# Kernel tuning notes

Hardware: AMD Instinct MI355X
Metric: run time of the kernel (lower is better)

The kernel has to match this reference:

```python
import jax, jax.numpy as jnp
import numpy as np

NG, NPG, EPG = 64, 256, 2048        # graphs, nodes/graph, edges/graph
N, E = NG * NPG, NG * EPG
FN, FE, FG = 256, 64, 128           # node/edge/global feature dims
MSG_DIMS = [FE + 2 * FN + FG, 512, 512, 256]   # message_arch '512-512-256'
UPD_DIMS = [256 + FN + FG, 512, 256]           # node_arch '512-256'
N_EMB_G, OUT_NODE, OUT_ACT = 256, 64, 8


def _mlp(x, params):
    # Linear -> ReLU stack (Dropout is identity in eval mode)
    for w, b in params:
        x = jax.nn.relu(x @ w + b)
    return x


def setup_inputs():
    key = jax.random.key(0)
    ks = jax.random.split(key, 24)
    nodes = jax.random.normal(ks[0], (N, FN), jnp.float32)
    edge_attr = jax.random.normal(ks[1], (E, FE), jnp.float32)
    global_attr = jax.random.normal(ks[2], (NG, FG), jnp.float32)
    # edges are grouped by graph (matches repeat_interleave(global, num_edges))
    rng = np.random.default_rng(0)
    gid_e = np.repeat(np.arange(NG), EPG)
    src = gid_e * NPG + rng.integers(0, NPG, E)
    tgt = gid_e * NPG + rng.integers(0, NPG, E)
    edge_indices = jnp.asarray(np.stack([src, tgt]), jnp.int32)
    num_nodes = jnp.full((NG,), NPG, jnp.int32)
    num_edges = jnp.full((NG,), EPG, jnp.int32)
    batch_indices = jnp.asarray(np.repeat(np.arange(NG), NPG), jnp.int32)

    def lin(k, fi, fo):
        kw, kb = jax.random.split(k)
        lim = 1.0 / np.sqrt(fi)
        return (jax.random.uniform(kw, (fi, fo), jnp.float32, -lim, lim),
                jax.random.uniform(kb, (fo,), jnp.float32, -lim, lim))

    inp = dict(nodes=nodes, edge_attr=edge_attr, global_attr=global_attr,
               edge_indices=edge_indices, num_nodes=num_nodes,
               num_edges=num_edges, batch_indices=batch_indices)
    for i in range(3):
        w, b = lin(ks[3 + i], MSG_DIMS[i], MSG_DIMS[i + 1])
        inp[f'msg_w{i}'], inp[f'msg_b{i}'] = w, b
    for i in range(2):
        w, b = lin(ks[6 + i], UPD_DIMS[i], UPD_DIMS[i + 1])
        inp[f'upd_w{i}'], inp[f'upd_b{i}'] = w, b
    inp['glob_w'], inp['glob_b'] = lin(ks[8], UPD_DIMS[-1] + FG, N_EMB_G)
    inp['emb_w'], inp['emb_b'] = lin(ks[9], UPD_DIMS[-1], OUT_NODE)
    inp['act_w'], inp['act_b'] = lin(ks[10], N_EMB_G, OUT_ACT)
    return inp


def reference(nodes, edge_attr, global_attr, edge_indices, num_nodes,
              num_edges, batch_indices, msg_w0, msg_b0, msg_w1, msg_b1,
              msg_w2, msg_b2, upd_w0, upd_b0, upd_w1, upd_b1,
              glob_w, glob_b, emb_w, emb_b, act_w, act_b):
    n, e = nodes.shape[0], edge_indices.shape[1]
    ng = global_attr.shape[0]
    src, tgt = edge_indices[0], edge_indices[1]
    glob_e = jnp.repeat(global_attr, num_edges, axis=0, total_repeat_length=e)
    concat = jnp.concatenate([nodes[src], edge_attr, nodes[tgt], glob_e], axis=1)
    # message_nn ends with ReLU; outer F.relu is a no-op on non-neg values
    message = _mlp(concat, [(msg_w0, msg_b0), (msg_w1, msg_b1), (msg_w2, msg_b2)])
    # scatter_max into per-node slots; messages >= 0 so zeros init matches fill=0
    aggr = jnp.zeros((n, message.shape[1]), message.dtype).at[tgt].max(message)
    glob_n = jnp.repeat(global_attr, num_nodes, axis=0, total_repeat_length=n)
    h = _mlp(jnp.concatenate([nodes, aggr, glob_n], axis=1),
             [(upd_w0, upd_b0), (upd_w1, upd_b1)])
    agg_nodes = jnp.zeros((ng, h.shape[1]), h.dtype).at[batch_indices].max(h)
    g = jax.nn.relu(jnp.concatenate([agg_nodes, global_attr], axis=1) @ glob_w + glob_b)
    node_pred = jax.nn.relu(h @ emb_w + emb_b)
    action = jax.nn.softmax(g @ act_w + act_b, axis=1)
    return node_pred, action
```

## Files before the change

kernel.cpp:

```cpp
#include <hip/hip_runtime.h>
#include <hip/hip_bf16.h>

typedef unsigned short u16;
using u16x4 = __attribute__((ext_vector_type(4))) unsigned short;
using u16x8 = __attribute__((ext_vector_type(8))) unsigned short;
using u32x4 = __attribute__((ext_vector_type(4))) unsigned int;
using f32x4 = __attribute__((ext_vector_type(4))) float;
using bf16x8 = __attribute__((ext_vector_type(8))) __bf16;

#define TNG 64
#define TNN 16384
#define TNE 131072
#define TFN 256
#define TFE 64
#define TFG 128

__device__ __forceinline__ u16 f2bf(float f) {
    unsigned u = __float_as_uint(f);
    unsigned r = (u + 0x7FFFu + ((u >> 16) & 1u)) >> 16;
    return (u16)r;
}
__device__ __forceinline__ float b2f(u16 h) {
    return __uint_as_float(((unsigned)h) << 16);
}

__device__ __forceinline__ void gload_lds16(const u16* g, u16* l) {
    __builtin_amdgcn_global_load_lds(
        (const __attribute__((address_space(1))) void*)g,
        (__attribute__((address_space(3))) void*)l, 16, 0, 0);
}

__device__ __forceinline__ int xcd_swz(int bid, int nwg) {
    return (nwg & 7) == 0 ? (bid & 7) * (nwg >> 3) + (bid >> 3) : bid;
}


__global__ void cast_kernel(const float* __restrict__ in, u16* __restrict__ out, int n4) {
    int i = blockIdx.x * 256 + threadIdx.x;
    if (i >= n4) return;
    f32x4 v = *(const f32x4*)(in + (size_t)i * 4);
    u16x4 o;
    o.x = f2bf(v.x); o.y = f2bf(v.y); o.z = f2bf(v.z); o.w = f2bf(v.w);
    *(u16x4*)(out + (size_t)i * 4) = o;
}


struct PrepTab {
    const float* W[8];
    int out_off[8];
    int Nin[8], Nact[8], r0[8], Ksub[8];
    int tile0[8];
    int tkn[8];
};

__global__ __launch_bounds__(256) void prep_weights_kernel(PrepTab tab, u16* __restrict__ wsbase) {
    const int b = blockIdx.x;
    int i = 7;
#pragma unroll
    for (int j = 7; j > 0; --j)
        if (b < tab.tile0[j]) i = j - 1;
    const int loc = b - tab.tile0[i];
    const int tk = loc % tab.tkn[i];
    const int tn = loc / tab.tkn[i];
    const int kb = tk * 64, nb = tn * 64;
    const int Nin = tab.Nin[i], Nact = tab.Nact[i], r0 = tab.r0[i], Ksub = tab.Ksub[i];
    const float* W = tab.W[i];
    u16* outp = wsbase + tab.out_off[i];

    __shared__ float t[64][65];
    const int tid = threadIdx.x;
    const int nl = tid & 63;
    const bool nok = (nb + nl) < Nact;
#pragma unroll 4
    for (int kk = tid >> 6; kk < 64; kk += 4) {
        float v = nok ? W[(size_t)(r0 + kb + kk) * Nin + nb + nl] : 0.0f;
        t[kk][nl] = v;
    }
    __syncthreads();
    const int kl = tid & 63;
#pragma unroll 4
    for (int nn = tid >> 6; nn < 64; nn += 4)
        outp[(size_t)(nb + nn) * Ksub + kb + kl] = f2bf(t[kl][nn]);
}


template <int K, int NXSH, bool RELU, bool OUT_BF16>
__global__ __launch_bounds__(256) void gemm_bt_kernel(
    const u16* __restrict__ A, const u16* __restrict__ Bt,
    const float* __restrict__ bias, void* __restrict__ Cv,
    int Nout, int ldc) {
    constexpr int NT = K / 32;
    __shared__ u16 As[4][4096];
    __shared__ u16 Bs[4][4096];
    const int w = xcd_swz(blockIdx.x, gridDim.x);
    const int bxi = w & ((1 << NXSH) - 1);
    const int byi = w >> NXSH;
    const int tid = threadIdx.x;
    const int wave = tid >> 6, lane = tid & 63;
    const int wr = wave >> 1, wc = wave & 1;
    const size_t brow = (size_t)byi * 128;
    const size_t bcol = (size_t)bxi * 128;
    const int srow = tid >> 2;
    const int qsrc = (tid & 3) ^ ((srow >> 1) & 3);
    const u16* aSrc = A + (brow + srow) * (size_t)K + qsrc * 8;
    const u16* bSrc = Bt + (bcol + srow) * (size_t)K + qsrc * 8;
    const size_t stepRows = (size_t)64 * K;

    auto stage = [&](int t, int buf) {
        const int k0 = t * 32;
        gload_lds16(aSrc + k0, &As[buf][tid * 8]);
        gload_lds16(aSrc + stepRows + k0, &As[buf][tid * 8 + 2048]);
        gload_lds16(bSrc + k0, &Bs[buf][tid * 8]);
        gload_lds16(bSrc + stepRows + k0, &Bs[buf][tid * 8 + 2048]);
    };

    f32x4 acc[4][4] = {};

    stage(0, 0);
    stage(1, 1);
    stage(2, 2);
#pragma unroll
    for (int t = 0; t < NT; ++t) {
        const int cur = t & 3;
        if (t + 2 < NT)      asm volatile("s_waitcnt vmcnt(8)" ::: "memory");
        else if (t + 1 < NT) asm volatile("s_waitcnt vmcnt(4)" ::: "memory");
        else                 asm volatile("s_waitcnt vmcnt(0)" ::: "memory");
        __builtin_amdgcn_s_barrier();
        if (t + 3 < NT) stage(t + 3, (t + 3) & 3);
        bf16x8 af[4], bfv[4];
#pragma unroll
        for (int m = 0; m < 4; ++m) {
            const int row = wr * 64 + m * 16 + (lane & 15);
            const int slot = (lane >> 4) ^ ((row >> 1) & 3);
            af[m] = *(const bf16x8*)&As[cur][row * 32 + slot * 8];
        }
#pragma unroll
        for (int n = 0; n < 4; ++n) {
            const int row = wc * 64 + n * 16 + (lane & 15);
            const int slot = (lane >> 4) ^ ((row >> 1) & 3);
            bfv[n] = *(const bf16x8*)&Bs[cur][row * 32 + slot * 8];
        }
#pragma unroll
        for (int m = 0; m < 4; ++m)
#pragma unroll
            for (int n = 0; n < 4; ++n)
                acc[m][n] = __builtin_amdgcn_mfma_f32_16x16x32_bf16(af[m], bfv[n], acc[m][n], 0, 0, 0);
    }

    const int rowSub = wr * 64 + (lane >> 4) * 4;
#pragma unroll
    for (int n = 0; n < 4; ++n) {
        const int col = (int)bcol + wc * 64 + n * 16 + (lane & 15);
        if (col >= Nout) continue;
        const float bv = bias ? bias[col] : 0.0f;
#pragma unroll
        for (int m = 0; m < 4; ++m) {
#pragma unroll
            for (int i = 0; i < 4; ++i) {
                float v = acc[m][n][i] + bv;
                if (RELU) v = fmaxf(v, 0.0f);
                size_t off = (brow + rowSub + m * 16 + i) * (size_t)ldc + col;
                if (OUT_BF16) ((u16*)Cv)[off] = f2bf(v);
                else ((float*)Cv)[off] = v;
            }
        }
    }
}


__global__ __launch_bounds__(256) void gemm_u0_kernel(
    const u16* __restrict__ nodes_bf, const u16* __restrict__ aggr,
    const u16* __restrict__ glob_bf, const u16* __restrict__ U0T,
    const float* __restrict__ bias, u16* __restrict__ C) {
    constexpr int NT = 20;
    __shared__ u16 As[4][4096];
    __shared__ u16 Bs[4][4096];
    const int w = xcd_swz(blockIdx.x, gridDim.x);
    const int bxi = w & 3;
    const int byi = w >> 2;
    const int tid = threadIdx.x;
    const int wave = tid >> 6, lane = tid & 63;
    const int wr = wave >> 1, wc = wave & 1;
    const size_t brow = (size_t)byi * 128;
    const size_t bcol = (size_t)bxi * 128;
    const int srow = tid >> 2;
    const int scol = ((tid & 3) ^ ((srow >> 1) & 3)) * 8;
    const int r0i = (int)brow + srow;
    const u16* bSrc = U0T + (bcol + srow) * (size_t)640 + scol;

    auto stage = [&](int t, int buf) {
        const int k0 = t * 32;
        const u16 *p0, *p1;
        if (k0 < 256) {
            p0 = nodes_bf + (size_t)r0i * 256 + k0 + scol;
            p1 = nodes_bf + (size_t)(r0i + 64) * 256 + k0 + scol;
        } else if (k0 < 512) {
            p0 = aggr + (size_t)r0i * 256 + (k0 - 256) + scol;
            p1 = aggr + (size_t)(r0i + 64) * 256 + (k0 - 256) + scol;
        } else {
            p0 = glob_bf + (size_t)(r0i >> 8) * 128 + (k0 - 512) + scol;
            p1 = glob_bf + (size_t)((r0i + 64) >> 8) * 128 + (k0 - 512) + scol;
        }
        gload_lds16(p0, &As[buf][tid * 8]);
        gload_lds16(p1, &As[buf][tid * 8 + 2048]);
        gload_lds16(bSrc + k0, &Bs[buf][tid * 8]);
        gload_lds16(bSrc + (size_t)64 * 640 + k0, &Bs[buf][tid * 8 + 2048]);
    };

    f32x4 acc[4][4] = {};

    stage(0, 0);
    stage(1, 1);
    stage(2, 2);
#pragma unroll
    for (int t = 0; t < NT; ++t) {
        const int cur = t & 3;
        if (t + 2 < NT)      asm volatile("s_waitcnt vmcnt(8)" ::: "memory");
        else if (t + 1 < NT) asm volatile("s_waitcnt vmcnt(4)" ::: "memory");
        else                 asm volatile("s_waitcnt vmcnt(0)" ::: "memory");
        __builtin_amdgcn_s_barrier();
        if (t + 3 < NT) stage(t + 3, (t + 3) & 3);
        bf16x8 af[4], bfv[4];
#pragma unroll
        for (int m = 0; m < 4; ++m) {
            const int row = wr * 64 + m * 16 + (lane & 15);
            const int slot = (lane >> 4) ^ ((row >> 1) & 3);
            af[m] = *(const bf16x8*)&As[cur][row * 32 + slot * 8];
        }
#pragma unroll
        for (int n = 0; n < 4; ++n) {
            const int row = wc * 64 + n * 16 + (lane & 15);
            const int slot = (lane >> 4) ^ ((row >> 1) & 3);
            bfv[n] = *(const bf16x8*)&Bs[cur][row * 32 + slot * 8];
        }
#pragma unroll
        for (int m = 0; m < 4; ++m)
#pragma unroll
            for (int n = 0; n < 4; ++n)
                acc[m][n] = __builtin_amdgcn_mfma_f32_16x16x32_bf16(af[m], bfv[n], acc[m][n], 0, 0, 0);
    }

    const int rowSub = wr * 64 + (lane >> 4) * 4;
#pragma unroll
    for (int n = 0; n < 4; ++n) {
        const int col = (int)bcol + wc * 64 + n * 16 + (lane & 15);
        const float bv = bias[col];
#pragma unroll
        for (int m = 0; m < 4; ++m)
#pragma unroll
            for (int i = 0; i < 4; ++i) {
                float v = fmaxf(acc[m][n][i] + bv, 0.0f);
                C[(brow + rowSub + m * 16 + i) * (size_t)512 + col] = f2bf(v);
            }
    }
}


__global__ __launch_bounds__(256) void gd_kernel(const float* __restrict__ glob,
                                                 const float* __restrict__ msg_w0,
                                                 const float* __restrict__ b0,
                                                 float* __restrict__ Gdb,
                                                 u16* __restrict__ glob_bf) {
    int g = blockIdx.x;
    __shared__ float in[TFG];
    if (threadIdx.x < TFG) {
        float v = glob[g * TFG + threadIdx.x];
        in[threadIdx.x] = v;
        glob_bf[g * TFG + threadIdx.x] = f2bf(v);
    }
    __syncthreads();
    for (int j = threadIdx.x; j < 512; j += 256) {
        float s = b0[j];
        for (int k = 0; k < TFG; ++k) s += in[k] * msg_w0[(size_t)(576 + k) * 512 + j];
        Gdb[(size_t)g * 512 + j] = s;
    }
}


__global__ __launch_bounds__(256) void h1_fused_kernel(
    const float* __restrict__ Ef, const u16* __restrict__ WbT,
    const u16* __restrict__ Pac, const float* __restrict__ Gdb,
    const int* __restrict__ src, const int* __restrict__ tgt,
    u16* __restrict__ h1, int e0) {
    __shared__ u16 smem[17408];
    u16* As = smem;
    u16* Bs = smem + 8192;
    const int w = xcd_swz(blockIdx.x, gridDim.x);
    const int bxi = w & 3;
    const int byi = w >> 2;
    const int tid = threadIdx.x;
    const int wave = tid >> 6, lane = tid & 63;
    const int wr = wave >> 1, wc = wave & 1;
    const int brow = byi * 128;
    const int bcol = bxi * 128;

    {
        const int r = tid >> 2;
        const int cq = (tid & 3) * 2;
        const int sw = r & 7;
#pragma unroll
        for (int h = 0; h < 2; ++h) {
            const float* sp = Ef + (size_t)(e0 + brow + r + h * 64) * 64 + cq * 8;
            f32x4 v0 = *(const f32x4*)(sp);
            f32x4 v1 = *(const f32x4*)(sp + 4);
            f32x4 v2 = *(const f32x4*)(sp + 8);
            f32x4 v3 = *(const f32x4*)(sp + 12);
            u16x8 o0, o1;
            o0[0] = f2bf(v0.x); o0[1] = f2bf(v0.y); o0[2] = f2bf(v0.z); o0[3] = f2bf(v0.w);
            o0[4] = f2bf(v1.x); o0[5] = f2bf(v1.y); o0[6] = f2bf(v1.z); o0[7] = f2bf(v1.w);
            o1[0] = f2bf(v2.x); o1[1] = f2bf(v2.y); o1[2] = f2bf(v2.z); o1[3] = f2bf(v2.w);
            o1[4] = f2bf(v3.x); o1[5] = f2bf(v3.y); o1[6] = f2bf(v3.z); o1[7] = f2bf(v3.w);
            *(u16x8*)&As[(r + h * 64) * 64 + (cq ^ sw) * 8] = o0;
            *(u16x8*)&As[(r + h * 64) * 64 + ((cq + 1) ^ sw) * 8] = o1;
        }
#pragma unroll
        for (int j = 0; j < 4; ++j) {
            int li = j * 256 + tid;
            int row = li >> 3;
            int gslot = (li & 7) ^ (row & 7);
            gload_lds16(WbT + (size_t)(bcol + row) * 64 + gslot * 8, &Bs[li * 8]);
        }
    }
    __syncthreads();

    f32x4 acc[4][4] = {};
#pragma unroll
    for (int k0 = 0; k0 < 64; k0 += 32) {
        bf16x8 af[4], bv[4];
#pragma unroll
        for (int m = 0; m < 4; ++m) {
            const int row = wr * 64 + m * 16 + (lane & 15);
            const int slot = ((k0 >> 3) + (lane >> 4)) ^ (row & 7);
            af[m] = *(const bf16x8*)&As[row * 64 + slot * 8];
        }
#pragma unroll
        for (int n = 0; n < 4; ++n) {
            const int row = wc * 64 + n * 16 + (lane & 15);
            const int slot = ((k0 >> 3) + (lane >> 4)) ^ (row & 7);
            bv[n] = *(const bf16x8*)&Bs[row * 64 + slot * 8];
        }
#pragma unroll
        for (int m = 0; m < 4; ++m)
#pragma unroll
            for (int n = 0; n < 4; ++n)
                acc[m][n] = __builtin_amdgcn_mfma_f32_16x16x32_bf16(af[m], bv[n], acc[m][n], 0, 0, 0);
    }
    __syncthreads();

    const int rowSub = wr * 64 + (lane >> 4) * 4;
#pragma unroll
    for (int m = 0; m < 4; ++m)
#pragma unroll
        for (int n = 0; n < 4; ++n)
#pragma unroll
            for (int i = 0; i < 4; ++i)
                smem[(rowSub + m * 16 + i) * 136 + wc * 64 + n * 16 + (lane & 15)] =
                    f2bf(acc[m][n][i]);
    __syncthreads();

#pragma unroll
    for (int it = 0; it < 8; ++it) {
        int lin = it * 256 + tid;
        int r = lin >> 4;
        int q = (lin & 15) * 8;
        int e = e0 + brow + r;
        int s = src[e];
        int t = tgt[e];
        int g = e >> 11;
        int col = bcol + q;
        u16x8 pa = *(const u16x8*)(Pac + (size_t)s * 1024 + col);
        u16x8 pc = *(const u16x8*)(Pac + (size_t)t * 1024 + 512 + col);
        u16x8 eb = *(const u16x8*)&smem[r * 136 + q];
        f32x4 g0 = *(const f32x4*)(Gdb + (size_t)g * 512 + col);
        f32x4 g1 = *(const f32x4*)(Gdb + (size_t)g * 512 + col + 4);
        u16x8 o;
#pragma unroll
        for (int j = 0; j < 8; ++j) {
            float gd = (j < 4) ? g0[j] : g1[j - 4];
            float v = b2f(pa[j]) + b2f(pc[j]) + b2f(eb[j]) + gd;
            o[j] = f2bf(fmaxf(v, 0.0f));
        }
        *(u16x8*)(h1 + (size_t)(brow + r) * 512 + col) = o;
    }
}


__global__ __launch_bounds__(1024) void scatter_max_kernel(
    const u16* __restrict__ msg, const int* __restrict__ tgt,
    u16* __restrict__ aggr) {
    int g = blockIdx.x >> 2;
    int fc = blockIdx.x & 3;
    __shared__ unsigned smax[256 * 64];
    int tid = threadIdx.x;
    for (int i = tid; i < 256 * 64; i += 1024) smax[i] = 0u;
    __syncthreads();
    const int eg = g * 2048;
    const int n0 = g * 256;
    const int f4 = (tid & 15) * 4;
    const int elane = tid >> 4;
    const u16* mbase = msg + fc * 64 + f4;
#pragma unroll
    for (int wv = 0; wv < 32; wv += 4) {
        const int e = eg + elane + wv * 64;
        int t0 = tgt[e], t1 = tgt[e + 64], t2 = tgt[e + 128], t3 = tgt[e + 192];
        u16x4 m0 = *(const u16x4*)(mbase + (size_t)e * 256);
        u16x4 m1 = *(const u16x4*)(mbase + (size_t)(e + 64) * 256);
        u16x4 m2 = *(const u16x4*)(mbase + (size_t)(e + 128) * 256);
        u16x4 m3 = *(const u16x4*)(mbase + (size_t)(e + 192) * 256);
        int a0 = t0 - n0, a1 = t1 - n0, a2 = t2 - n0, a3 = t3 - n0;
        if ((unsigned)a0 < 256u) {
            atomicMax(&smax[a0 * 64 + f4],     ((unsigned)m0.x) << 16);
            atomicMax(&smax[a0 * 64 + f4 + 1], ((unsigned)m0.y) << 16);
            atomicMax(&smax[a0 * 64 + f4 + 2], ((unsigned)m0.z) << 16);
            atomicMax(&smax[a0 * 64 + f4 + 3], ((unsigned)m0.w) << 16);
        }
        if ((unsigned)a1 < 256u) {
            atomicMax(&smax[a1 * 64 + f4],     ((unsigned)m1.x) << 16);
            atomicMax(&smax[a1 * 64 + f4 + 1], ((unsigned)m1.y) << 16);
            atomicMax(&smax[a1 * 64 + f4 + 2], ((unsigned)m1.z) << 16);
            atomicMax(&smax[a1 * 64 + f4 + 3], ((unsigned)m1.w) << 16);
        }
        if ((unsigned)a2 < 256u) {
            atomicMax(&smax[a2 * 64 + f4],     ((unsigned)m2.x) << 16);
            atomicMax(&smax[a2 * 64 + f4 + 1], ((unsigned)m2.y) << 16);
            atomicMax(&smax[a2 * 64 + f4 + 2], ((unsigned)m2.z) << 16);
            atomicMax(&smax[a2 * 64 + f4 + 3], ((unsigned)m2.w) << 16);
        }
        if ((unsigned)a3 < 256u) {
            atomicMax(&smax[a3 * 64 + f4],     ((unsigned)m3.x) << 16);
            atomicMax(&smax[a3 * 64 + f4 + 1], ((unsigned)m3.y) << 16);
            atomicMax(&smax[a3 * 64 + f4 + 2], ((unsigned)m3.z) << 16);
            atomicMax(&smax[a3 * 64 + f4 + 3], ((unsigned)m3.w) << 16);
        }
    }
    __syncthreads();
    for (int i = tid; i < 256 * 64; i += 1024) {
        int nl = i >> 6, ff = i & 63;
        aggr[(size_t)(n0 + nl) * 256 + fc * 64 + ff] = (u16)(smax[nl * 64 + ff] >> 16);
    }
}


__global__ __launch_bounds__(256) void head_kernel(
    const u16* __restrict__ h, const float* __restrict__ glob,
    const float* __restrict__ W, const float* __restrict__ b,
    const float* __restrict__ actw, const float* __restrict__ actb,
    float* __restrict__ out_act) {
    int g = blockIdx.x;
    int tid = threadIdx.x;
    __shared__ float in[384];
    __shared__ float go[256];
    __shared__ float logits[8];
    {
        const size_t base = (size_t)g * 256 * 256 + tid;
        float m0 = 0.0f, m1 = 0.0f, m2 = 0.0f, m3 = 0.0f;
        for (int n = 0; n < 256; n += 4) {
            m0 = fmaxf(m0, b2f(h[base + (size_t)n * 256]));
            m1 = fmaxf(m1, b2f(h[base + (size_t)(n + 1) * 256]));
            m2 = fmaxf(m2, b2f(h[base + (size_t)(n + 2) * 256]));
            m3 = fmaxf(m3, b2f(h[base + (size_t)(n + 3) * 256]));
        }
        in[tid] = fmaxf(fmaxf(m0, m1), fmaxf(m2, m3));
        if (tid < 128) in[256 + tid] = glob[(size_t)g * 128 + tid];
    }
    __syncthreads();
    {
        float s = b[tid];
        for (int k = 0; k < 384; ++k) s += in[k] * W[(size_t)k * 256 + tid];
        go[tid] = fmaxf(s, 0.0f);
    }
    __syncthreads();
    if (tid < 8) {
        float s = actb[tid];
        for (int k = 0; k < 256; ++k) s += go[k] * actw[(size_t)k * 8 + tid];
        logits[tid] = s;
    }
    __syncthreads();
    if (tid == 0) {
        float mx = logits[0];
        for (int i = 1; i < 8; ++i) mx = fmaxf(mx, logits[i]);
        float ex[8], den = 0.0f;
        for (int i = 0; i < 8; ++i) { ex[i] = expf(logits[i] - mx); den += ex[i]; }
        float inv = 1.0f / den;
        for (int i = 0; i < 8; ++i) out_act[(size_t)g * 8 + i] = ex[i] * inv;
    }
}


constexpr size_t OFF_NODES_BF = 0;
constexpr size_t OFF_GLOB_BF  = OFF_NODES_BF + (size_t)TNN * TFN * 2;
constexpr size_t OFF_WACT = OFF_GLOB_BF + (size_t)TNG * TFG * 2;
constexpr size_t OFF_WBT  = OFF_WACT + 1024 * 256 * 2;
constexpr size_t OFF_W1T  = OFF_WBT + 512 * 64 * 2;
constexpr size_t OFF_W2T  = OFF_W1T + 512 * 512 * 2;
constexpr size_t OFF_U0T  = OFF_W2T + 256 * 512 * 2;
constexpr size_t OFF_U1T  = OFF_U0T + 512 * 640 * 2;
constexpr size_t OFF_EMBT = OFF_U1T + 256 * 512 * 2;
constexpr size_t OFF_AGGR = OFF_EMBT + 128 * 256 * 2;
constexpr size_t OFF_GDB  = OFF_AGGR + (size_t)TNN * 256 * 2;
constexpr size_t OFF_PAC  = OFF_GDB + 64 * 512 * 4;
constexpr size_t OFF_MSG  = OFF_PAC + (size_t)TNN * 1024 * 2;
constexpr size_t OFF_V    = OFF_MSG + (size_t)TNE * 256 * 2;
constexpr size_t SZ_HU1   = (size_t)TNN * 512 * 2;

extern "C" void kernel_launch(void* const* d_in, const int* in_sizes, int n_in,
                              void* d_out, int out_size, void* d_ws, size_t ws_size,
                              hipStream_t stream) {
    const float* nodes       = (const float*)d_in[0];
    const float* edge_attr   = (const float*)d_in[1];
    const float* global_attr = (const float*)d_in[2];
    const int*   edge_idx    = (const int*)d_in[3];
    const float* msg_w0 = (const float*)d_in[7];
    const float* msg_b0 = (const float*)d_in[8];
    const float* msg_w1 = (const float*)d_in[9];
    const float* msg_b1 = (const float*)d_in[10];
    const float* msg_w2 = (const float*)d_in[11];
    const float* msg_b2 = (const float*)d_in[12];
    const float* upd_w0 = (const float*)d_in[13];
    const float* upd_b0 = (const float*)d_in[14];
    const float* upd_w1 = (const float*)d_in[15];
    const float* upd_b1 = (const float*)d_in[16];
    const float* glob_w = (const float*)d_in[17];
    const float* glob_b = (const float*)d_in[18];
    const float* emb_w  = (const float*)d_in[19];
    const float* emb_b  = (const float*)d_in[20];
    const float* act_w  = (const float*)d_in[21];
    const float* act_b  = (const float*)d_in[22];

    const int* src = edge_idx;
    const int* tgt = edge_idx + TNE;

    char* ws = (char*)d_ws;
    u16* nodes_bf = (u16*)(ws + OFF_NODES_BF);
    u16* glob_bf  = (u16*)(ws + OFF_GLOB_BF);
    u16* WacT = (u16*)(ws + OFF_WACT);
    u16* WbT  = (u16*)(ws + OFF_WBT);
    u16* W1T  = (u16*)(ws + OFF_W1T);
    u16* W2T  = (u16*)(ws + OFF_W2T);
    u16* U0T  = (u16*)(ws + OFF_U0T);
    u16* U1T  = (u16*)(ws + OFF_U1T);
    u16* EmbT = (u16*)(ws + OFF_EMBT);
    u16* aggr = (u16*)(ws + OFF_AGGR);
    float* Gdb = (float*)(ws + OFF_GDB);
    u16* Pac  = (u16*)(ws + OFF_PAC);
    u16* msgc = (u16*)(ws + OFF_MSG);
    float* out = (float*)d_out;

    size_t CH = 32768;
    while (CH > 2048 && OFF_V + CH * 2048 > ws_size) CH >>= 1;
    const int nchunk = (int)((size_t)TNE / CH);

    u16* h1c  = (u16*)(ws + OFF_V);
    u16* h2c  = (u16*)(ws + OFF_V + CH * 1024);
    u16* hu1  = (u16*)(ws + OFF_V);
    u16* h_bf = (u16*)(ws + OFF_AGGR);

    cast_kernel<<<(TNN * TFN / 4 + 255) / 256, 256, 0, stream>>>(nodes, nodes_bf, TNN * TFN / 4);

    PrepTab tab;
    int ntiles = 0;
    {
        const float* Ws[8]  = {msg_w0, msg_w0, msg_w0, msg_w1, msg_w2, upd_w0, upd_w1, emb_w};
        int offs[8] = {(int)(OFF_WACT / 2), (int)(OFF_WACT / 2) + 131072, (int)(OFF_WBT / 2),
                       (int)(OFF_W1T / 2), (int)(OFF_W2T / 2), (int)(OFF_U0T / 2),
                       (int)(OFF_U1T / 2), (int)(OFF_EMBT / 2)};
        int nin[8]  = {512, 512, 512, 512, 256, 512, 256, 64};
        int nact[8] = {512, 512, 512, 512, 256, 512, 256, 64};
        int r0v[8]  = {0, 320, 256, 0, 0, 0, 0, 0};
        int ksub[8] = {256, 256, 64, 512, 512, 640, 512, 256};
        int npad[8] = {512, 512, 512, 512, 256, 512, 256, 128};
        int acc = 0;
        for (int i = 0; i < 8; ++i) {
            tab.W[i] = Ws[i]; tab.out_off[i] = offs[i]; tab.Nin[i] = nin[i];
            tab.Nact[i] = nact[i]; tab.r0[i] = r0v[i]; tab.Ksub[i] = ksub[i];
            tab.tkn[i] = ksub[i] / 64;
            tab.tile0[i] = acc;
            acc += (npad[i] / 64) * (ksub[i] / 64);
        }
        ntiles = acc;
    }
    prep_weights_kernel<<<ntiles, 256, 0, stream>>>(tab, (u16*)ws);
    gd_kernel<<<64, 256, 0, stream>>>(global_attr, msg_w0, msg_b0, Gdb, glob_bf);

    gemm_bt_kernel<256, 3, false, true><<<1024, 256, 0, stream>>>(nodes_bf, WacT, nullptr, Pac, 1024, 1024);

    for (int ci = 0; ci < nchunk; ++ci) {
        const int e0 = (int)(ci * CH);
        const int nwg = (int)(CH / 32);
        h1_fused_kernel<<<nwg, 256, 0, stream>>>(
            edge_attr, WbT, Pac, Gdb, src, tgt, h1c, e0);
        gemm_bt_kernel<512, 2, true, true><<<nwg, 256, 0, stream>>>(h1c, W1T, msg_b1, h2c, 512, 512);
        gemm_bt_kernel<512, 1, true, true><<<nwg / 2, 256, 0, stream>>>(
            h2c, W2T, msg_b2, msgc + (size_t)e0 * 256, 256, 256);
    }
    scatter_max_kernel<<<TNG * 4, 1024, 0, stream>>>(msgc, tgt, aggr);

    gemm_u0_kernel<<<512, 256, 0, stream>>>(nodes_bf, aggr, glob_bf, U0T, upd_b0, hu1);
    gemm_bt_kernel<512, 1, true, true><<<256, 256, 0, stream>>>(hu1, U1T, upd_b1, h_bf, 256, 256);

    head_kernel<<<64, 256, 0, stream>>>(h_bf, global_attr, glob_w, glob_b,
                                        act_w, act_b, out + (size_t)TNN * 64);
    gemm_bt_kernel<256, 0, true, false><<<128, 256, 0, stream>>>(h_bf, EmbT, emb_b, out, 64, 64);

    (void)in_sizes; (void)n_in; (void)out_size;
}
```

Baseline: 345.4 us.

## Add 128x256-tile GEMM with triple-buffered LDS and use it for big GEMMs

Adds a GEMM variant whose 128x256 output tile is computed by four waves, each owning 128x64, with a three-stage LDS pipeline in place of four stages. It replaces the 128x128 kernel for the node projection, the two message MLP layers and the update layer, halving the grid sizes. The larger tile is meant to raise arithmetic intensity and cut A-operand reloads. The cost is 128 accumulator registers per lane, which may hurt occupancy, and fewer workgroups for the smaller GEMMs.

```diff
diff --git a/kernel.cpp b/kernel.cpp
--- a/kernel.cpp
+++ b/kernel.cpp
@@ -81,6 +81,88 @@
 #pragma unroll 4
     for (int nn = tid >> 6; nn < 64; nn += 4)
         outp[(size_t)(nb + nn) * Ksub + kb + kl] = f2bf(t[kl][nn]);
+}
+
+
+template <int K, int NXSH, bool RELU, bool OUT_BF16>
+__global__ __launch_bounds__(256, 2) void gemm_bt_wide_kernel(
+    const u16* __restrict__ A, const u16* __restrict__ Bt,
+    const float* __restrict__ bias, void* __restrict__ Cv,
+    int Nout, int ldc) {
+    constexpr int NT = K / 32;
+    __shared__ u16 As[3][4096];
+    __shared__ u16 Bs[3][8192];
+    const int w = xcd_swz(blockIdx.x, gridDim.x);
+    const int bxi = w & ((1 << NXSH) - 1);
+    const int byi = w >> NXSH;
+    const int tid = threadIdx.x;
+    const int wave = tid >> 6, lane = tid & 63;
+    const size_t brow = (size_t)byi * 128;
+    const size_t bcol = (size_t)bxi * 256;
+    const int srow = tid >> 2;
+    const int qsrc = (tid & 3) ^ ((srow >> 1) & 3);
+    const u16* aSrc = A + (brow + srow) * (size_t)K + qsrc * 8;
+    const u16* bSrc = Bt + (bcol + srow) * (size_t)K + qsrc * 8;
+    const size_t stepRows = (size_t)64 * K;
+
+    auto stage = [&](int t, int buf) {
+        const int k0 = t * 32;
+        gload_lds16(aSrc + k0, &As[buf][tid * 8]);
+        gload_lds16(aSrc + stepRows + k0, &As[buf][tid * 8 + 2048]);
+#pragma unroll
+        for (int j = 0; j < 4; ++j)
+            gload_lds16(bSrc + j * stepRows + k0, &Bs[buf][j * 2048 + tid * 8]);
+    };
+
+    f32x4 acc[8][4] = {};
+
+    stage(0, 0);
+    stage(1, 1);
+#pragma unroll
+    for (int t = 0; t < NT; ++t) {
+        const int cur = t % 3;
+        if (t + 1 < NT) asm volatile("s_waitcnt vmcnt(6)" ::: "memory");
+        else            asm volatile("s_waitcnt vmcnt(0)" ::: "memory");
+        __builtin_amdgcn_s_barrier();
+        if (t + 2 < NT) stage(t + 2, (t + 2) % 3);
+        bf16x8 af[8], bfv[4];
+#pragma unroll
+        for (int m = 0; m < 8; ++m) {
+            const int row = m * 16 + (lane & 15);
+            const int slot = (lane >> 4) ^ ((row >> 1) & 3);
+            af[m] = *(const bf16x8*)&As[cur][row * 32 + slot * 8];
+        }
+#pragma unroll
+        for (int n = 0; n < 4; ++n) {
+            const int row = wave * 64 + n * 16 + (lane & 15);
+            const int slot = (lane >> 4) ^ ((row >> 1) & 3);
+            bfv[n] = *(const bf16x8*)&Bs[cur][row * 32 + slot * 8];
+        }
+#pragma unroll
+        for (int m = 0; m < 8; ++m)
+#pragma unroll
+            for (int n = 0; n < 4; ++n)
+                acc[m][n] = __builtin_amdgcn_mfma_f32_16x16x32_bf16(af[m], bfv[n], acc[m][n], 0, 0, 0);
+    }
+
+    const int rowSub = (lane >> 4) * 4;
+#pragma unroll
+    for (int n = 0; n < 4; ++n) {
+        const int col = (int)bcol + wave * 64 + n * 16 + (lane & 15);
+        if (col >= Nout) continue;
+        const float bv = bias ? bias[col] : 0.0f;
+#pragma unroll
+        for (int m = 0; m < 8; ++m) {
+#pragma unroll
+            for (int i = 0; i < 4; ++i) {
+                float v = acc[m][n][i] + bv;
+                if (RELU) v = fmaxf(v, 0.0f);
+                size_t off = (brow + m * 16 + rowSub + i) * (size_t)ldc + col;
+                if (OUT_BF16) ((u16*)Cv)[off] = f2bf(v);
+                else ((float*)Cv)[off] = v;
+            }
+        }
+    }
 }
 
 
@@ -582,21 +664,22 @@
     prep_weights_kernel<<<ntiles, 256, 0, stream>>>(tab, (u16*)ws);
     gd_kernel<<<64, 256, 0, stream>>>(global_attr, msg_w0, msg_b0, Gdb, glob_bf);
 
-    gemm_bt_kernel<256, 3, false, true><<<1024, 256, 0, stream>>>(nodes_bf, WacT, nullptr, Pac, 1024, 1024);
+    gemm_bt_wide_kernel<256, 2, false, true><<<512, 256, 0, stream>>>(nodes_bf, WacT, nullptr, Pac, 1024, 1024);
 
     for (int ci = 0; ci < nchunk; ++ci) {
         const int e0 = (int)(ci * CH);
         const int nwg = (int)(CH / 32);
+        const int mb = (int)(CH / 128);
         h1_fused_kernel<<<nwg, 256, 0, stream>>>(
             edge_attr, WbT, Pac, Gdb, src, tgt, h1c, e0);
-        gemm_bt_kernel<512, 2, true, true><<<nwg, 256, 0, stream>>>(h1c, W1T, msg_b1, h2c, 512, 512);
-        gemm_bt_kernel<512, 1, true, true><<<nwg / 2, 256, 0, stream>>>(
+        gemm_bt_wide_kernel<512, 1, true, true><<<mb * 2, 256, 0, stream>>>(h1c, W1T, msg_b1, h2c, 512, 512);
+        gemm_bt_wide_kernel<512, 0, true, true><<<mb, 256, 0, stream>>>(
             h2c, W2T, msg_b2, msgc + (size_t)e0 * 256, 256, 256);
     }
     scatter_max_kernel<<<TNG * 4, 1024, 0, stream>>>(msgc, tgt, aggr);
 
     gemm_u0_kernel<<<512, 256, 0, stream>>>(nodes_bf, aggr, glob_bf, U0T, upd_b0, hu1);
-    gemm_bt_kernel<512, 1, true, true><<<256, 256, 0, stream>>>(hu1, U1T, upd_b1, h_bf, 256, 256);
+    gemm_bt_wide_kernel<512, 0, true, true><<<128, 256, 0, stream>>>(hu1, U1T, upd_b1, h_bf, 256, 256);
 
     head_kernel<<<64, 256, 0, stream>>>(h_bf, global_attr, glob_w, glob_b,
                                         act_w, act_b, out + (size_t)TNN * 64);
```

New measurement: 378.4 us. +9.5%, slower.

## Fuse final message GEMM with global atomic scatter-max into fp32 aggregate

Applied to the files above, without the earlier changes.

The last message-MLP GEMM now applies bias and ReLU and scatters results directly into a zeroed fp32 per-node buffer with global atomicMax. This replaces writing the bf16 message tensor and the separate LDS-based scatter_max kernel. It removes the message tensor round trip through memory, but adds a zero-fill kernel, a cast kernel, and many global atomics (one per output element) that may contend.

```diff
diff --git a/kernel.cpp b/kernel.cpp
--- a/kernel.cpp
+++ b/kernel.cpp
@@ -42,6 +42,12 @@
     u16x4 o;
     o.x = f2bf(v.x); o.y = f2bf(v.y); o.z = f2bf(v.z); o.w = f2bf(v.w);
     *(u16x4*)(out + (size_t)i * 4) = o;
+}
+
+
+__global__ void zero32_kernel(u32x4* __restrict__ p, int n) {
+    int i = blockIdx.x * 256 + threadIdx.x;
+    if (i < n) p[i] = (u32x4){0u, 0u, 0u, 0u};
 }
 
 
@@ -168,6 +174,92 @@
 }
 
 
+__global__ __launch_bounds__(256) void gemm_msg_scatter_kernel(
+    const u16* __restrict__ A, const u16* __restrict__ Bt,
+    const float* __restrict__ bias, unsigned* __restrict__ aggr32,
+    const int* __restrict__ tgt, int e0) {
+    constexpr int K = 512;
+    constexpr int NT = K / 32;
+    __shared__ u16 As[4][4096];
+    __shared__ u16 Bs[4][4096];
+    const int w = xcd_swz(blockIdx.x, gridDim.x);
+    const int bxi = w & 1;
+    const int byi = w >> 1;
+    const int tid = threadIdx.x;
+    const int wave = tid >> 6, lane = tid & 63;
+    const int wr = wave >> 1, wc = wave & 1;
+    const size_t brow = (size_t)byi * 128;
+    const size_t bcol = (size_t)bxi * 128;
+    const int srow = tid >> 2;
+    const int qsrc = (tid & 3) ^ ((srow >> 1) & 3);
+    const u16* aSrc = A + (brow + srow) * (size_t)K + qsrc * 8;
+    const u16* bSrc = Bt + (bcol + srow) * (size_t)K + qsrc * 8;
+    const size_t stepRows = (size_t)64 * K;
+
+    auto stage = [&](int t, int buf) {
+        const int k0 = t * 32;
+        gload_lds16(aSrc + k0, &As[buf][tid * 8]);
+        gload_lds16(aSrc + stepRows + k0, &As[buf][tid * 8 + 2048]);
+        gload_lds16(bSrc + k0, &Bs[buf][tid * 8]);
+        gload_lds16(bSrc + stepRows + k0, &Bs[buf][tid * 8 + 2048]);
+    };
+
+    f32x4 acc[4][4] = {};
+
+    stage(0, 0);
+    stage(1, 1);
+    stage(2, 2);
+#pragma unroll
+    for (int t = 0; t < NT; ++t) {
+        const int cur = t & 3;
+        if (t + 2 < NT)      asm volatile("s_waitcnt vmcnt(8)" ::: "memory");
+        else if (t + 1 < NT) asm volatile("s_waitcnt vmcnt(4)" ::: "memory");
+        else                 asm volatile("s_waitcnt vmcnt(0)" ::: "memory");
+        __builtin_amdgcn_s_barrier();
+        if (t + 3 < NT) stage(t + 3, (t + 3) & 3);
+        bf16x8 af[4], bfv[4];
+#pragma unroll
+        for (int m = 0; m < 4; ++m) {
+            const int row = wr * 64 + m * 16 + (lane & 15);
+            const int slot = (lane >> 4) ^ ((row >> 1) & 3);
+            af[m] = *(const bf16x8*)&As[cur][row * 32 + slot * 8];
+        }
+#pragma unroll
+        for (int n = 0; n < 4; ++n) {
+            const int row = wc * 64 + n * 16 + (lane & 15);
+            const int slot = (lane >> 4) ^ ((row >> 1) & 3);
+            bfv[n] = *(const bf16x8*)&Bs[cur][row * 32 + slot * 8];
+        }
+#pragma unroll
+        for (int m = 0; m < 4; ++m)
+#pragma unroll
+            for (int n = 0; n < 4; ++n)
+                acc[m][n] = __builtin_amdgcn_mfma_f32_16x16x32_bf16(af[m], bfv[n], acc[m][n], 0, 0, 0);
+    }
+
+    const int rowSub = wr * 64 + (lane >> 4) * 4;
+    float bv[4];
+#pragma unroll
+    for (int n = 0; n < 4; ++n)
+        bv[n] = bias[(int)bcol + wc * 64 + n * 16 + (lane & 15)];
+#pragma unroll
+    for (int m = 0; m < 4; ++m) {
+#pragma unroll
+        for (int i = 0; i < 4; ++i) {
+            const int rowL = (int)brow + rowSub + m * 16 + i;
+            const int node = tgt[e0 + rowL];
+            unsigned* base = aggr32 + (size_t)node * 256;
+#pragma unroll
+            for (int n = 0; n < 4; ++n) {
+                const int col = (int)bcol + wc * 64 + n * 16 + (lane & 15);
+                float v = fmaxf(acc[m][n][i] + bv[n], 0.0f);
+                atomicMax(base + col, __float_as_uint(v));
+            }
+        }
+    }
+}
+
+
 __global__ __launch_bounds__(256) void gemm_u0_kernel(
     const u16* __restrict__ nodes_bf, const u16* __restrict__ aggr,
     const u16* __restrict__ glob_bf, const u16* __restrict__ U0T,
@@ -385,59 +477,14 @@
 }
 
 
-__global__ __launch_bounds__(1024) void scatter_max_kernel(
-    const u16* __restrict__ msg, const int* __restrict__ tgt,
-    u16* __restrict__ aggr) {
-    int g = blockIdx.x >> 2;
-    int fc = blockIdx.x & 3;
-    __shared__ unsigned smax[256 * 64];
-    int tid = threadIdx.x;
-    for (int i = tid; i < 256 * 64; i += 1024) smax[i] = 0u;
-    __syncthreads();
-    const int eg = g * 2048;
-    const int n0 = g * 256;
-    const int f4 = (tid & 15) * 4;
-    const int elane = tid >> 4;
-    const u16* mbase = msg + fc * 64 + f4;
-#pragma unroll
-    for (int wv = 0; wv < 32; wv += 4) {
-        const int e = eg + elane + wv * 64;
-        int t0 = tgt[e], t1 = tgt[e + 64], t2 = tgt[e + 128], t3 = tgt[e + 192];
-        u16x4 m0 = *(const u16x4*)(mbase + (size_t)e * 256);
-        u16x4 m1 = *(const u16x4*)(mbase + (size_t)(e + 64) * 256);
-        u16x4 m2 = *(const u16x4*)(mbase + (size_t)(e + 128) * 256);
-        u16x4 m3 = *(const u16x4*)(mbase + (size_t)(e + 192) * 256);
-        int a0 = t0 - n0, a1 = t1 - n0, a2 = t2 - n0, a3 = t3 - n0;
-        if ((unsigned)a0 < 256u) {
-            atomicMax(&smax[a0 * 64 + f4],     ((unsigned)m0.x) << 16);
-            atomicMax(&smax[a0 * 64 + f4 + 1], ((unsigned)m0.y) << 16);
-            atomicMax(&smax[a0 * 64 + f4 + 2], ((unsigned)m0.z) << 16);
-            atomicMax(&smax[a0 * 64 + f4 + 3], ((unsigned)m0.w) << 16);
-        }
-        if ((unsigned)a1 < 256u) {
-            atomicMax(&smax[a1 * 64 + f4],     ((unsigned)m1.x) << 16);
-            atomicMax(&smax[a1 * 64 + f4 + 1], ((unsigned)m1.y) << 16);
-            atomicMax(&smax[a1 * 64 + f4 + 2], ((unsigned)m1.z) << 16);
-            atomicMax(&smax[a1 * 64 + f4 + 3], ((unsigned)m1.w) << 16);
-        }
-        if ((unsigned)a2 < 256u) {
-            atomicMax(&smax[a2 * 64 + f4],     ((unsigned)m2.x) << 16);
-            atomicMax(&smax[a2 * 64 + f4 + 1], ((unsigned)m2.y) << 16);
-            atomicMax(&smax[a2 * 64 + f4 + 2], ((unsigned)m2.z) << 16);
-            atomicMax(&smax[a2 * 64 + f4 + 3], ((unsigned)m2.w) << 16);
-        }
-        if ((unsigned)a3 < 256u) {
-            atomicMax(&smax[a3 * 64 + f4],     ((unsigned)m3.x) << 16);
-            atomicMax(&smax[a3 * 64 + f4 + 1], ((unsigned)m3.y) << 16);
-            atomicMax(&smax[a3 * 64 + f4 + 2], ((unsigned)m3.z) << 16);
-            atomicMax(&smax[a3 * 64 + f4 + 3], ((unsigned)m3.w) << 16);
-        }
-    }
-    __syncthreads();
-    for (int i = tid; i < 256 * 64; i += 1024) {
-        int nl = i >> 6, ff = i & 63;
-        aggr[(size_t)(n0 + nl) * 256 + fc * 64 + ff] = (u16)(smax[nl * 64 + ff] >> 16);
-    }
+__global__ void aggr_cast_kernel(const unsigned* __restrict__ in, u16* __restrict__ out, int n4) {
+    int i = blockIdx.x * 256 + threadIdx.x;
+    if (i >= n4) return;
+    u32x4 v = *(const u32x4*)(in + (size_t)i * 4);
+    u16x4 o;
+    o.x = f2bf(__uint_as_float(v.x)); o.y = f2bf(__uint_as_float(v.y));
+    o.z = f2bf(__uint_as_float(v.z)); o.w = f2bf(__uint_as_float(v.w));
+    *(u16x4*)(out + (size_t)i * 4) = o;
 }
 
 
@@ -499,8 +546,8 @@
 constexpr size_t OFF_AGGR = OFF_EMBT + 128 * 256 * 2;
 constexpr size_t OFF_GDB  = OFF_AGGR + (size_t)TNN * 256 * 2;
 constexpr size_t OFF_PAC  = OFF_GDB + 64 * 512 * 4;
-constexpr size_t OFF_MSG  = OFF_PAC + (size_t)TNN * 1024 * 2;
-constexpr size_t OFF_V    = OFF_MSG + (size_t)TNE * 256 * 2;
+constexpr size_t OFF_AG32 = OFF_PAC + (size_t)TNN * 1024 * 2;
+constexpr size_t OFF_V    = OFF_AG32 + (size_t)TNN * 256 * 4;
 constexpr size_t SZ_HU1   = (size_t)TNN * 512 * 2;
 
 extern "C" void kernel_launch(void* const* d_in, const int* in_sizes, int n_in,
@@ -543,7 +590,7 @@
     u16* aggr = (u16*)(ws + OFF_AGGR);
     float* Gdb = (float*)(ws + OFF_GDB);
     u16* Pac  = (u16*)(ws + OFF_PAC);
-    u16* msgc = (u16*)(ws + OFF_MSG);
+    unsigned* aggr32 = (unsigned*)(ws + OFF_AG32);
     float* out = (float*)d_out;
 
     size_t CH = 32768;
@@ -556,6 +603,7 @@
     u16* h_bf = (u16*)(ws + OFF_AGGR);
 
     cast_kernel<<<(TNN * TFN / 4 + 255) / 256, 256, 0, stream>>>(nodes, nodes_bf, TNN * TFN / 4);
+    zero32_kernel<<<(TNN * 256 / 4 + 255) / 256, 256, 0, stream>>>((u32x4*)aggr32, TNN * 256 / 4);
 
     PrepTab tab;
     int ntiles = 0;
@@ -590,10 +638,9 @@
         h1_fused_kernel<<<nwg, 256, 0, stream>>>(
             edge_attr, WbT, Pac, Gdb, src, tgt, h1c, e0);
         gemm_bt_kernel<512, 2, true, true><<<nwg, 256, 0, stream>>>(h1c, W1T, msg_b1, h2c, 512, 512);
-        gemm_bt_kernel<512, 1, true, true><<<nwg / 2, 256, 0, stream>>>(
-            h2c, W2T, msg_b2, msgc + (size_t)e0 * 256, 256, 256);
-    }
-    scatter_max_kernel<<<TNG * 4, 1024, 0, stream>>>(msgc, tgt, aggr);
+        gemm_msg_scatter_kernel<<<nwg / 2, 256, 0, stream>>>(h2c, W2T, msg_b2, aggr32, tgt, e0);
+    }
+    aggr_cast_kernel<<<(TNN * 256 / 4 + 255) / 256, 256, 0, stream>>>(aggr32, aggr, TNN * 256 / 4);
 
     gemm_u0_kernel<<<512, 256, 0, stream>>>(nodes_bf, aggr, glob_bf, U0T, upd_b0, hu1);
     gemm_bt_kernel<512, 1, true, true><<<256, 256, 0, stream>>>(hu1, U1T, upd_b1, h_bf, 256, 256);
```

Measured after the change: 401.2 us. 1.16x slower.
